# Performance work log

Hardware: AMD Instinct MI355X
Metric: run time of the kernel (lower is better)

## Reference

```python
import jax, jax.numpy as jnp
import numpy as np

SQRT_HALF = np.float32(np.sqrt(0.5))


def _weight_norm(v, g):
    # torch weight_norm dim=0: per-output-row normalization, w = g * v / ||v||_row
    return (g / jnp.linalg.norm(v, axis=1))[:, None] * v


def setup_inputs() -> dict:
    key = jax.random.key(0)
    ks = jax.random.split(key, 6)
    B, L, C, E, H, W = 32, 1024, 1024, 1024, 14, 14
    return {
        "x": jax.random.normal(ks[0], (B, L, C), dtype=jnp.float32),
        "word_embed": jax.random.normal(ks[1], (B, L, E), dtype=jnp.float32),
        "conv_feats": jax.random.normal(ks[2], (B, E, H, W), dtype=jnp.float32),
        "in_v": jax.random.normal(ks[3], (E, C), dtype=jnp.float32) * np.float32(1.0 / np.sqrt(C)),
        "in_g": jnp.ones((E,), dtype=jnp.float32),
        "in_b": jnp.zeros((E,), dtype=jnp.float32),
        "out_v": jax.random.normal(ks[4], (C, E), dtype=jnp.float32) * np.float32(1.0 / np.sqrt(E)),
        "out_g": jnp.ones((C,), dtype=jnp.float32),
        "out_b": jnp.zeros((C,), dtype=jnp.float32),
    }


def reference(x, word_embed, conv_feats, in_v, in_g, in_b, out_v, out_g, out_b):
    # in_projection (weight-normed linear) + word_embed, scaled
    Wi = _weight_norm(in_v, in_g)                      # [E, C]
    h = (jnp.einsum('blc,ec->ble', x, Wi) + in_b + word_embed) * SQRT_HALF  # [B, L, E]

    B, E, H, W = conv_feats.shape
    n = H * W
    y = conv_feats.reshape(B, E, n)                    # [B, E, n]
    scores = jnp.einsum('ble,bev->blv', h, y)          # [B, L, n]
    attn = jax.nn.softmax(scores, axis=-1)             # [B, L, n]
    ctx = jnp.einsum('blv,bev->ble', attn, y)          # [B, L, E]
    ctx = ctx * jnp.asarray(n * np.sqrt(1.0 / n), dtype=ctx.dtype)  # = sqrt(n)

    # out_projection + residual, scaled
    Wo = _weight_norm(out_v, out_g)                    # [C, E]
    out = (jnp.einsum('ble,ce->blc', ctx, Wo) + out_b + x) * SQRT_HALF  # [B, L, C]
    return out, attn
```

## Files before the change

### kernel.cpp

```cpp
#include <hip/hip_runtime.h>
#include <hip/hip_bf16.h>

typedef unsigned short u16;
typedef __bf16 bf16x8 __attribute__((ext_vector_type(8)));
typedef _Float16 f16x8 __attribute__((ext_vector_type(8)));
typedef unsigned short u16x8 __attribute__((ext_vector_type(8)));
typedef float f32x4 __attribute__((ext_vector_type(4)));

#define SQHF 0.70710678118654752440f

__device__ __forceinline__ u16 f2bf(float f) {
  __hip_bfloat16 h = __float2bfloat16(f);
  return __builtin_bit_cast(u16, h);
}
__device__ __forceinline__ float bf2f(u16 u) {
  unsigned x = ((unsigned)u) << 16;
  return __builtin_bit_cast(float, x);
}
__device__ __forceinline__ void split2(float v, u16& hi, u16& lo) {
  hi = f2bf(v);
  lo = f2bf(v - bf2f(hi));
}

template <int N>
__device__ __forceinline__ void vmwait() {
  asm volatile("s_waitcnt vmcnt(%0)" ::"i"(N) : "memory");
}

__device__ __forceinline__ void gload_lds16(const void* g, void* l) {
  __builtin_amdgcn_global_load_lds(
      (const __attribute__((address_space(1))) unsigned int*)g,
      (__attribute__((address_space(3))) unsigned int*)l, 16, 0, 0);
}

__device__ __forceinline__ float block_sum(float v) {
#pragma unroll
  for (int o = 32; o; o >>= 1) v += __shfl_xor(v, o);
  __shared__ float red[4];
  if ((threadIdx.x & 63) == 0) red[threadIdx.x >> 6] = v;
  __syncthreads();
  return red[0] + red[1] + red[2] + red[3];
}

__global__ void wnorm_t_kernel(const float* __restrict__ v, const float* __restrict__ g,
                               u16* __restrict__ wth, u16* __restrict__ wtl) {
  const int e = blockIdx.x;
  const float* vr = v + (long)e * 1024;
  float ss = 0.f;
  for (int c = threadIdx.x; c < 1024; c += 256) { float t = vr[c]; ss += t * t; }
  const float tot = block_sum(ss);
  const float scl = g[e] / sqrtf(tot);
  for (int c = threadIdx.x; c < 1024; c += 256) {
    u16 hi, lo;
    split2(vr[c] * scl, hi, lo);
    wth[(long)c * 1024 + e] = hi;
    wtl[(long)c * 1024 + e] = lo;
  }
}

__global__ void wnorm_kernel(const float* __restrict__ v, const float* __restrict__ g,
                             u16* __restrict__ w) {
  const int c = blockIdx.x;
  const float* vr = v + (long)c * 1024;
  float ss = 0.f;
  for (int e = threadIdx.x; e < 1024; e += 256) { float t = vr[e]; ss += t * t; }
  const float tot = block_sum(ss);
  const float scl = g[c] / sqrtf(tot);
  for (int e = threadIdx.x; e < 1024; e += 256) w[(long)c * 1024 + e] = f2bf(vr[e] * scl);
}

__global__ void prep_y_kernel(const float* __restrict__ conv, u16* __restrict__ bth,
                              u16* __restrict__ btl, u16* __restrict__ concat) {
  const int b = blockIdx.x >> 4;
  const int e0 = (blockIdx.x & 15) << 6;
  __shared__ float tile[64 * 224];
  const float* cb = conv + ((long)b * 1024 + e0) * 196;
  for (int idx = threadIdx.x; idx < 64 * 224; idx += 256) {
    const int rr = idx / 224, vv = idx - rr * 224;
    tile[idx] = (vv < 196) ? cb[(long)rr * 196 + vv] : 0.f;
  }
  __syncthreads();
  for (int idx = threadIdx.x; idx < 256 * 64; idx += 256) {
    const int vr = idx >> 6, c = idx & 63;
    const float val = (vr < 224) ? tile[c * 224 + vr] : 0.f;
    u16 hi, lo;
    split2(val, hi, lo);
    const long o = ((long)b * 256 + vr) * 1024 + e0 + c;
    bth[o] = hi;
    btl[o] = lo;
    const _Float16 hf = (_Float16)val;
    concat[((long)b * 256 + vr) * 2048 + 1024 + e0 + c] = __builtin_bit_cast(u16, hf);
  }
}

__global__ void rc_kernel(const float* __restrict__ in_b, const u16* __restrict__ bth,
                          const u16* __restrict__ btl, float* __restrict__ rc) {
  const int b = blockIdx.x / 49;
  const int v = (blockIdx.x % 49) * 4 + (threadIdx.x >> 6);
  const int lane = threadIdx.x & 63;
  const long base = ((long)b * 256 + v) * 1024;
  float acc = 0.f;
  for (int e = lane; e < 1024; e += 64)
    acc += in_b[e] * (bf2f(bth[base + e]) + bf2f(btl[base + e]));
#pragma unroll
  for (int o = 32; o; o >>= 1) acc += __shfl_xor(acc, o);
  if (lane == 0) rc[b * 256 + v] = acc;
}

__global__ void softmax_kernel(const float* __restrict__ s0b, const float* __restrict__ s1b,
                               const float* __restrict__ rc,
                               float* __restrict__ attn, u16* __restrict__ attn_bf) {
  const long row = (long)blockIdx.x * 4 + (threadIdx.x >> 6);
  const int lane = threadIdx.x & 63;
  const int b = (int)(row >> 10);
  const float* s0 = s0b + row * 256;
  const float* s1 = s1b + row * 256;
  const float* rcb = rc + b * 256;
  float v0 = (s0[lane] + s1[lane] + rcb[lane]) * SQHF;
  float v1 = (s0[64 + lane] + s1[64 + lane] + rcb[64 + lane]) * SQHF;
  float v2 = (s0[128 + lane] + s1[128 + lane] + rcb[128 + lane]) * SQHF;
  float v3 = (lane < 4) ? (s0[192 + lane] + s1[192 + lane] + rcb[192 + lane]) * SQHF : -1e30f;
  float mx = fmaxf(fmaxf(v0, v1), fmaxf(v2, v3));
#pragma unroll
  for (int o = 32; o; o >>= 1) mx = fmaxf(mx, __shfl_xor(mx, o));
  const float e0 = __expf(v0 - mx), e1 = __expf(v1 - mx), e2 = __expf(v2 - mx);
  const float e3 = (lane < 4) ? __expf(v3 - mx) : 0.f;
  float sm = e0 + e1 + e2 + e3;
#pragma unroll
  for (int o = 32; o; o >>= 1) sm += __shfl_xor(sm, o);
  const float inv = 1.f / sm;
  float* arow = attn + row * 196;
  arow[lane] = e0 * inv;
  arow[64 + lane] = e1 * inv;
  arow[128 + lane] = e2 * inv;
  if (lane < 4) arow[192 + lane] = e3 * inv;
  u16* brow = attn_bf + row * 256;
  brow[lane] = f2bf(e0 * inv);
  brow[64 + lane] = f2bf(e1 * inv);
  brow[128 + lane] = f2bf(e2 * inv);
  brow[192 + lane] = (lane < 4) ? f2bf(e3 * inv) : (u16)0;
}

template <int EPI, int MODE>
__global__ __launch_bounds__(256) void gemm128(
    const u16* __restrict__ Ah, const u16* __restrict__ Al,
    const float* __restrict__ Af0, const float* __restrict__ Af1, int kSw,
    const u16* __restrict__ Bh, const u16* __restrict__ Bl,
    int N, int K, int ldA, int ldB, int ldOut,
    int mTilesPerBatch, long bStride, int aTilesMod, int kSplit2,
    const float* __restrict__ bias, const float* __restrict__ extra,
    float scale, void* __restrict__ out1, void* __restrict__ out2) {
  constexpr int SPLIT = (MODE == 1);
  constexpr int AF16 = (MODE == 2);
  constexpr int DEPTH = AF16 ? 3 : 2;
  constexpr int LPS = (MODE == 0) ? 4 : (MODE == 1 ? 8 : 6);
  constexpr int TAL = 4096;
  constexpr int TBH = (MODE == 0) ? 4096 : 8192;
  constexpr int TBL = 12288;
  constexpr int HSM = (MODE == 0) ? 8192 : (MODE == 1 ? 16384 : 12288);
  __shared__ __align__(16) u16 smem[HSM * DEPTH];

  int bid = blockIdx.x, nwg = gridDim.x, half = 0;
  if (kSplit2) { half = bid & 1; bid >>= 1; nwg >>= 1; }
  const int kOff = half << 10;

  const int numN = N >> 7;
  const int q = nwg >> 3, r = nwg & 7, xcd = bid & 7, l8 = bid >> 3;
  const int wg = (xcd < r ? xcd * (q + 1) : r * (q + 1) + (xcd - r) * q) + l8;
  const int mTile = wg / numN, nTile = wg - mTile * numN;
  const long rowBase = (long)mTile << 7;
  const int colBase = nTile << 7;
  const int aTile = aTilesMod ? (mTile % aTilesMod) : mTile;
  const long aRowBase = (long)aTile << 7;
  const long bOff = mTilesPerBatch ? (long)(mTile / mTilesPerBatch) * bStride : 0;

  const u16* Agh = AF16 ? nullptr : (Ah + aRowBase * ldA);
  const u16* Agl = SPLIT ? (Al + aRowBase * ldA) : nullptr;
  const u16* Bgh = Bh + bOff + (long)colBase * ldB;
  const u16* Bgl = SPLIT ? (Bl + bOff + (long)colBase * ldB) : nullptr;

  const int tid = threadIdx.x;
  const int wave = tid >> 6, lane = tid & 63;
  const int wr = wave >> 1, wc = wave & 1;
  const int sr = wave * 16 + (lane >> 2);
  const int scS = (((lane & 3) ^ ((sr >> 1) & 3)) << 3);
  const int lr = lane & 15;
  const int lk = (lane >> 4) << 3;

  f32x4 acc[4][4];
#pragma unroll
  for (int m = 0; m < 4; ++m)
#pragma unroll
    for (int n = 0; n < 4; ++n) acc[m][n] = f32x4{0.f, 0.f, 0.f, 0.f};

  auto stage = [&](int buf, int k0) {
    u16* sb = smem + buf * HSM;
    if (AF16) {
      const int gk = k0 + kOff;
      const float* As = (gk < kSw) ? (Af0 + aRowBase * (long)ldA + gk)
                                   : (Af1 + aRowBase * (long)ldA + (gk - kSw));
      const int rr = tid >> 3;
#pragma unroll
      for (int i = 0; i < 4; ++i) {
        const int row = i * 32 + rr;
        const int csw = (((tid & 7) ^ (row & 7)) << 2);
        gload_lds16(As + (long)row * ldA + csw, &sb[i * 2048 + wave * 512]);
      }
#pragma unroll
      for (int i = 0; i < 2; ++i) {
        const long ro = (long)(i * 64 + sr) * ldB + k0 + kOff + scS;
        gload_lds16(Bgh + ro, &sb[TBH + i * 2048 + wave * 512]);
      }
    } else {
#pragma unroll
      for (int i = 0; i < 2; ++i) {
        const long roA = (long)(i * 64 + sr) * ldA + k0 + scS;
        const long roB = (long)(i * 64 + sr) * ldB + k0 + scS;
        const int lo_ = i * 2048 + wave * 512;
        gload_lds16(Agh + roA, &sb[lo_]);
        gload_lds16(Bgh + roB, &sb[TBH + lo_]);
        if (SPLIT) {
          gload_lds16(Agl + roA, &sb[TAL + lo_]);
          gload_lds16(Bgl + roB, &sb[TBL + lo_]);
        }
      }
    }
  };

  auto compute = [&](int buf) {
    const u16* sb = smem + buf * HSM;
    if (AF16) {
      f16x8 fa[4], fb[4];
      const char* smemb = (const char*)sb;
#pragma unroll
      for (int m = 0; m < 4; ++m) {
        const int row = wr * 64 + m * 16 + lr;
        const int xr = (row & 7) << 4;
        const char* rp = smemb + row * 128;
        const f32x4 p0 = *(const f32x4*)(rp + ((lk << 2) ^ xr));
        const f32x4 p1 = *(const f32x4*)(rp + (((lk << 2) + 16) ^ xr));
        f16x8 va;
        va[0] = (_Float16)p0.x; va[1] = (_Float16)p0.y;
        va[2] = (_Float16)p0.z; va[3] = (_Float16)p0.w;
        va[4] = (_Float16)p1.x; va[5] = (_Float16)p1.y;
        va[6] = (_Float16)p1.z; va[7] = (_Float16)p1.w;
        fa[m] = va;
      }
#pragma unroll
      for (int n = 0; n < 4; ++n) {
        const int row = wc * 64 + n * 16 + lr;
        const int off = row * 32 + (((lane >> 4) ^ ((row >> 1) & 3)) << 3);
        fb[n] = __builtin_bit_cast(f16x8, *(const u16x8*)&sb[TBH + off]);
      }
      __builtin_amdgcn_s_setprio(1);
#pragma unroll
      for (int m = 0; m < 4; ++m)
#pragma unroll
        for (int n = 0; n < 4; ++n)
          acc[m][n] = __builtin_amdgcn_mfma_f32_16x16x32_f16(fa[m], fb[n], acc[m][n], 0, 0, 0);
      __builtin_amdgcn_s_setprio(0);
    } else {
      bf16x8 fah[4], fbh[4], fal[4], fbl[4];
#pragma unroll
      for (int m = 0; m < 4; ++m) {
        const int row = wr * 64 + m * 16 + lr;
        const int off = row * 32 + (((lane >> 4) ^ ((row >> 1) & 3)) << 3);
        fah[m] = __builtin_bit_cast(bf16x8, *(const u16x8*)&sb[off]);
        if (SPLIT) fal[m] = __builtin_bit_cast(bf16x8, *(const u16x8*)&sb[TAL + off]);
      }
#pragma unroll
      for (int n = 0; n < 4; ++n) {
        const int row = wc * 64 + n * 16 + lr;
        const int off = row * 32 + (((lane >> 4) ^ ((row >> 1) & 3)) << 3);
        fbh[n] = __builtin_bit_cast(bf16x8, *(const u16x8*)&sb[TBH + off]);
        if (SPLIT) fbl[n] = __builtin_bit_cast(bf16x8, *(const u16x8*)&sb[TBL + off]);
      }
#pragma unroll
      for (int m = 0; m < 4; ++m)
#pragma unroll
        for (int n = 0; n < 4; ++n) {
          acc[m][n] = __builtin_amdgcn_mfma_f32_16x16x32_bf16(fah[m], fbh[n], acc[m][n], 0, 0, 0);
          if (SPLIT) {
            acc[m][n] = __builtin_amdgcn_mfma_f32_16x16x32_bf16(fah[m], fbl[n], acc[m][n], 0, 0, 0);
            acc[m][n] = __builtin_amdgcn_mfma_f32_16x16x32_bf16(fal[m], fbh[n], acc[m][n], 0, 0, 0);
          }
        }
    }
  };

  const int nSteps = K >> 5;
  stage(0, 0);
  if (DEPTH == 3 && nSteps > 1) stage(1, 32);
  for (int t = 0; t < nSteps; ++t) {
    const int cur = t % DEPTH;
    if (t + DEPTH - 1 < nSteps) {
      stage((t + DEPTH - 1) % DEPTH, (t + DEPTH - 1) << 5);
      vmwait<LPS * (DEPTH - 1)>();
    } else if (DEPTH == 3 && t + 1 < nSteps) {
      vmwait<LPS>();
    } else {
      vmwait<0>();
    }
    __builtin_amdgcn_s_barrier();
    __builtin_amdgcn_sched_barrier(0);
    compute(cur);
    __builtin_amdgcn_sched_barrier(0);
    __builtin_amdgcn_s_barrier();
  }

  const int rloc = (lane >> 4) << 2;
  float* o3 = (float*)(half ? out2 : out1);
#pragma unroll
  for (int m = 0; m < 4; ++m) {
#pragma unroll
    for (int n = 0; n < 4; ++n) {
      const int col = colBase + wc * 64 + n * 16 + lr;
#pragma unroll
      for (int j = 0; j < 4; ++j) {
        const long row = rowBase + wr * 64 + m * 16 + rloc + j;
        const float v = acc[m][n][j];
        if (EPI == 1) {
          ((float*)out1)[row * (long)ldOut + col] =
              (v + bias[col] + extra[row * 1024 + col]) * scale;
        } else if (EPI == 2) {
          ((u16*)out1)[row * (long)ldOut + col] = f2bf(v * scale);
        } else if (EPI == 3) {
          o3[row * (long)ldOut + col] = v;
        } else if (EPI == 6) {
          const _Float16 hv = (_Float16)v;
          ((u16*)out1)[row * (long)ldOut + col] = __builtin_bit_cast(u16, hv);
        }
      }
    }
  }
}

extern "C" void kernel_launch(void* const* d_in, const int* in_sizes, int n_in,
                              void* d_out, int out_size, void* d_ws, size_t ws_size,
                              hipStream_t stream) {
  (void)in_sizes; (void)n_in; (void)out_size; (void)ws_size;
  const float* x     = (const float*)d_in[0];
  const float* we    = (const float*)d_in[1];
  const float* conv  = (const float*)d_in[2];
  const float* in_v  = (const float*)d_in[3];
  const float* in_g  = (const float*)d_in[4];
  const float* in_b  = (const float*)d_in[5];
  const float* out_v = (const float*)d_in[6];
  const float* out_g = (const float*)d_in[7];
  const float* out_b = (const float*)d_in[8];
  float* out  = (float*)d_out;
  float* attn = out + 33554432l;

  char* ws = (char*)d_ws;
  u16* bth    = (u16*)(ws);
  u16* btl    = (u16*)(ws + 16777216l);
  u16* concat = (u16*)(ws + 33554432l);
  u16* wth    = (u16*)(ws + 67108864l);
  u16* wtl    = (u16*)(ws + 69206016l);
  u16* wo     = (u16*)(ws + 71303168l);
  u16* zo     = (u16*)(ws + 73400320l);
  u16* attbf  = (u16*)(ws + 90177536l);
  float* rc   = (float*)(ws + 106954752l);
  float* s1   = (float*)(ws + 109051904l);
  float* s0   = out;

  wnorm_t_kernel<<<1024, 256, 0, stream>>>(in_v, in_g, wth, wtl);
  wnorm_kernel<<<1024, 256, 0, stream>>>(out_v, out_g, wo);
  prep_y_kernel<<<512, 256, 0, stream>>>(conv, bth, btl, concat);
  rc_kernel<<<1568, 256, 0, stream>>>(in_b, bth, btl, rc);
  gemm128<6, 1><<<512, 256, 0, stream>>>(
      bth, btl, nullptr, nullptr, 0, wth, wtl,
      1024, 1024, 1024, 1024, 2048, 0, 0, 0, 0, nullptr, nullptr, 1.f, concat, nullptr);
  gemm128<3, 2><<<1024, 256, 0, stream>>>(
      nullptr, nullptr, x, we, 1024, concat, nullptr,
      256, 1024, 1024, 2048, 256, 8, 524288l, 0, 1, nullptr, nullptr, 1.f, s0, s1);
  softmax_kernel<<<8192, 256, 0, stream>>>(s0, s1, rc, attn, attbf);
  gemm128<2, 0><<<512, 256, 0, stream>>>(
      wo, nullptr, nullptr, nullptr, 0, bth, nullptr,
      256, 1024, 1024, 1024, 256, 8, 262144l, 8, 0, nullptr, nullptr, 14.f, zo, nullptr);
  gemm128<1, 0><<<2048, 256, 0, stream>>>(
      attbf, nullptr, nullptr, nullptr, 0, zo, nullptr,
      1024, 256, 256, 256, 1024, 8, 262144l, 0, 0, out_b, x, SQHF, out, nullptr);
}
```

Baseline: 355.6 us.

## Switch all GEMMs to single-pass fp16 and fuse rc into prep kernel

Replaces the three-pass split-bf16 (hi/lo) emulation of fp32 in the y·Wi GEMM with a single fp16 MFMA pass. It also moves the remaining bf16 GEMMs to fp16 operands and reads the fp16 copy of conv features from the concat buffer, which drops the separate bth/btl buffers. The rc bias-dot kernel is folded into prep_y, accumulating with atomics into a zero-initialised buffer. This cuts MFMA work, memory traffic and one launch, at the cost of lower precision in the h-projection path and fp16 range risk.

Measured after the change: 302.1 us. 15.1% less time.

```diff
diff --git a/kernel.cpp b/kernel.cpp
--- a/kernel.cpp
+++ b/kernel.cpp
@@ -2,24 +2,15 @@
 #include <hip/hip_bf16.h>
 
 typedef unsigned short u16;
-typedef __bf16 bf16x8 __attribute__((ext_vector_type(8)));
 typedef _Float16 f16x8 __attribute__((ext_vector_type(8)));
 typedef unsigned short u16x8 __attribute__((ext_vector_type(8)));
 typedef float f32x4 __attribute__((ext_vector_type(4)));
 
 #define SQHF 0.70710678118654752440f
 
-__device__ __forceinline__ u16 f2bf(float f) {
-  __hip_bfloat16 h = __float2bfloat16(f);
+__device__ __forceinline__ u16 f2h(float f) {
+  const _Float16 h = (_Float16)f;
   return __builtin_bit_cast(u16, h);
-}
-__device__ __forceinline__ float bf2f(u16 u) {
-  unsigned x = ((unsigned)u) << 16;
-  return __builtin_bit_cast(float, x);
-}
-__device__ __forceinline__ void split2(float v, u16& hi, u16& lo) {
-  hi = f2bf(v);
-  lo = f2bf(v - bf2f(hi));
 }
 
 template <int N>
@@ -43,19 +34,14 @@
 }
 
 __global__ void wnorm_t_kernel(const float* __restrict__ v, const float* __restrict__ g,
-                               u16* __restrict__ wth, u16* __restrict__ wtl) {
+                               u16* __restrict__ wtf) {
   const int e = blockIdx.x;
   const float* vr = v + (long)e * 1024;
   float ss = 0.f;
   for (int c = threadIdx.x; c < 1024; c += 256) { float t = vr[c]; ss += t * t; }
   const float tot = block_sum(ss);
   const float scl = g[e] / sqrtf(tot);
-  for (int c = threadIdx.x; c < 1024; c += 256) {
-    u16 hi, lo;
-    split2(vr[c] * scl, hi, lo);
-    wth[(long)c * 1024 + e] = hi;
-    wtl[(long)c * 1024 + e] = lo;
-  }
+  for (int c = threadIdx.x; c < 1024; c += 256) wtf[(long)c * 1024 + e] = f2h(vr[c] * scl);
 }
 
 __global__ void wnorm_kernel(const float* __restrict__ v, const float* __restrict__ g,
@@ -66,11 +52,11 @@
   for (int e = threadIdx.x; e < 1024; e += 256) { float t = vr[e]; ss += t * t; }
   const float tot = block_sum(ss);
   const float scl = g[c] / sqrtf(tot);
-  for (int e = threadIdx.x; e < 1024; e += 256) w[(long)c * 1024 + e] = f2bf(vr[e] * scl);
-}
-
-__global__ void prep_y_kernel(const float* __restrict__ conv, u16* __restrict__ bth,
-                              u16* __restrict__ btl, u16* __restrict__ concat) {
+  for (int e = threadIdx.x; e < 1024; e += 256) w[(long)c * 1024 + e] = f2h(vr[e] * scl);
+}
+
+__global__ void prep_y_kernel(const float* __restrict__ conv, const float* __restrict__ in_b,
+                              u16* __restrict__ concat, float* __restrict__ rc) {
   const int b = blockIdx.x >> 4;
   const int e0 = (blockIdx.x & 15) << 6;
   __shared__ float tile[64 * 224];
@@ -83,33 +69,20 @@
   for (int idx = threadIdx.x; idx < 256 * 64; idx += 256) {
     const int vr = idx >> 6, c = idx & 63;
     const float val = (vr < 224) ? tile[c * 224 + vr] : 0.f;
-    u16 hi, lo;
-    split2(val, hi, lo);
-    const long o = ((long)b * 256 + vr) * 1024 + e0 + c;
-    bth[o] = hi;
-    btl[o] = lo;
-    const _Float16 hf = (_Float16)val;
-    concat[((long)b * 256 + vr) * 2048 + 1024 + e0 + c] = __builtin_bit_cast(u16, hf);
-  }
-}
-
-__global__ void rc_kernel(const float* __restrict__ in_b, const u16* __restrict__ bth,
-                          const u16* __restrict__ btl, float* __restrict__ rc) {
-  const int b = blockIdx.x / 49;
-  const int v = (blockIdx.x % 49) * 4 + (threadIdx.x >> 6);
-  const int lane = threadIdx.x & 63;
-  const long base = ((long)b * 256 + v) * 1024;
-  float acc = 0.f;
-  for (int e = lane; e < 1024; e += 64)
-    acc += in_b[e] * (bf2f(bth[base + e]) + bf2f(btl[base + e]));
-#pragma unroll
-  for (int o = 32; o; o >>= 1) acc += __shfl_xor(acc, o);
-  if (lane == 0) rc[b * 256 + v] = acc;
+    concat[((long)b * 256 + vr) * 2048 + 1024 + e0 + c] = f2h(val);
+  }
+  const int v = threadIdx.x;
+  if (v < 196) {
+    float s = 0.f;
+#pragma unroll 8
+    for (int rr = 0; rr < 64; ++rr) s += in_b[e0 + rr] * tile[rr * 224 + v];
+    atomicAdd(&rc[b * 256 + v], s);
+  }
 }
 
 __global__ void softmax_kernel(const float* __restrict__ s0b, const float* __restrict__ s1b,
                                const float* __restrict__ rc,
-                               float* __restrict__ attn, u16* __restrict__ attn_bf) {
+                               float* __restrict__ attn, u16* __restrict__ attn_f) {
   const long row = (long)blockIdx.x * 4 + (threadIdx.x >> 6);
   const int lane = threadIdx.x & 63;
   const int b = (int)(row >> 10);
@@ -134,31 +107,27 @@
   arow[64 + lane] = e1 * inv;
   arow[128 + lane] = e2 * inv;
   if (lane < 4) arow[192 + lane] = e3 * inv;
-  u16* brow = attn_bf + row * 256;
-  brow[lane] = f2bf(e0 * inv);
-  brow[64 + lane] = f2bf(e1 * inv);
-  brow[128 + lane] = f2bf(e2 * inv);
-  brow[192 + lane] = (lane < 4) ? f2bf(e3 * inv) : (u16)0;
+  u16* brow = attn_f + row * 256;
+  brow[lane] = f2h(e0 * inv);
+  brow[64 + lane] = f2h(e1 * inv);
+  brow[128 + lane] = f2h(e2 * inv);
+  brow[192 + lane] = (lane < 4) ? f2h(e3 * inv) : (u16)0;
 }
 
 template <int EPI, int MODE>
 __global__ __launch_bounds__(256) void gemm128(
-    const u16* __restrict__ Ah, const u16* __restrict__ Al,
+    const u16* __restrict__ Ah,
     const float* __restrict__ Af0, const float* __restrict__ Af1, int kSw,
-    const u16* __restrict__ Bh, const u16* __restrict__ Bl,
+    const u16* __restrict__ Bh,
     int N, int K, int ldA, int ldB, int ldOut,
     int mTilesPerBatch, long bStride, int aTilesMod, int kSplit2,
     const float* __restrict__ bias, const float* __restrict__ extra,
     float scale, void* __restrict__ out1, void* __restrict__ out2) {
-  constexpr int SPLIT = (MODE == 1);
-  constexpr int AF16 = (MODE == 2);
-  constexpr int DEPTH = AF16 ? 3 : 2;
-  constexpr int LPS = (MODE == 0) ? 4 : (MODE == 1 ? 8 : 6);
-  constexpr int TAL = 4096;
-  constexpr int TBH = (MODE == 0) ? 4096 : 8192;
-  constexpr int TBL = 12288;
-  constexpr int HSM = (MODE == 0) ? 8192 : (MODE == 1 ? 16384 : 12288);
-  __shared__ __align__(16) u16 smem[HSM * DEPTH];
+  constexpr int AF32 = (MODE == 2);
+  constexpr int LPS = AF32 ? 6 : 4;
+  constexpr int TBH = AF32 ? 8192 : 4096;
+  constexpr int HSM = AF32 ? 12288 : 8192;
+  __shared__ __align__(16) u16 smem[HSM * 2];
 
   int bid = blockIdx.x, nwg = gridDim.x, half = 0;
   if (kSplit2) { half = bid & 1; bid >>= 1; nwg >>= 1; }
@@ -174,10 +143,8 @@
   const long aRowBase = (long)aTile << 7;
   const long bOff = mTilesPerBatch ? (long)(mTile / mTilesPerBatch) * bStride : 0;
 
-  const u16* Agh = AF16 ? nullptr : (Ah + aRowBase * ldA);
-  const u16* Agl = SPLIT ? (Al + aRowBase * ldA) : nullptr;
+  const u16* Agh = AF32 ? nullptr : (Ah + aRowBase * ldA);
   const u16* Bgh = Bh + bOff + (long)colBase * ldB;
-  const u16* Bgl = SPLIT ? (Bl + bOff + (long)colBase * ldB) : nullptr;
 
   const int tid = threadIdx.x;
   const int wave = tid >> 6, lane = tid & 63;
@@ -195,7 +162,7 @@
 
   auto stage = [&](int buf, int k0) {
     u16* sb = smem + buf * HSM;
-    if (AF16) {
+    if (AF32) {
       const int gk = k0 + kOff;
       const float* As = (gk < kSw) ? (Af0 + aRowBase * (long)ldA + gk)
                                    : (Af1 + aRowBase * (long)ldA + (gk - kSw));
@@ -214,23 +181,19 @@
     } else {
 #pragma unroll
       for (int i = 0; i < 2; ++i) {
-        const long roA = (long)(i * 64 + sr) * ldA + k0 + scS;
-        const long roB = (long)(i * 64 + sr) * ldB + k0 + scS;
+        const long roA = (long)(i * 64 + sr) * ldA + k0 + kOff + scS;
+        const long roB = (long)(i * 64 + sr) * ldB + k0 + kOff + scS;
         const int lo_ = i * 2048 + wave * 512;
         gload_lds16(Agh + roA, &sb[lo_]);
         gload_lds16(Bgh + roB, &sb[TBH + lo_]);
-        if (SPLIT) {
-          gload_lds16(Agl + roA, &sb[TAL + lo_]);
-          gload_lds16(Bgl + roB, &sb[TBL + lo_]);
-        }
       }
     }
   };
 
   auto compute = [&](int buf) {
     const u16* sb = smem + buf * HSM;
-    if (AF16) {
-      f16x8 fa[4], fb[4];
+    f16x8 fa[4], fb[4];
+    if (AF32) {
       const char* smemb = (const char*)sb;
 #pragma unroll
       for (int m = 0; m < 4; ++m) {
@@ -246,57 +209,35 @@
         va[6] = (_Float16)p1.z; va[7] = (_Float16)p1.w;
         fa[m] = va;
       }
-#pragma unroll
-      for (int n = 0; n < 4; ++n) {
-        const int row = wc * 64 + n * 16 + lr;
-        const int off = row * 32 + (((lane >> 4) ^ ((row >> 1) & 3)) << 3);
-        fb[n] = __builtin_bit_cast(f16x8, *(const u16x8*)&sb[TBH + off]);
-      }
-      __builtin_amdgcn_s_setprio(1);
-#pragma unroll
-      for (int m = 0; m < 4; ++m)
-#pragma unroll
-        for (int n = 0; n < 4; ++n)
-          acc[m][n] = __builtin_amdgcn_mfma_f32_16x16x32_f16(fa[m], fb[n], acc[m][n], 0, 0, 0);
-      __builtin_amdgcn_s_setprio(0);
     } else {
-      bf16x8 fah[4], fbh[4], fal[4], fbl[4];
 #pragma unroll
       for (int m = 0; m < 4; ++m) {
         const int row = wr * 64 + m * 16 + lr;
         const int off = row * 32 + (((lane >> 4) ^ ((row >> 1) & 3)) << 3);
-        fah[m] = __builtin_bit_cast(bf16x8, *(const u16x8*)&sb[off]);
-        if (SPLIT) fal[m] = __builtin_bit_cast(bf16x8, *(const u16x8*)&sb[TAL + off]);
-      }
-#pragma unroll
-      for (int n = 0; n < 4; ++n) {
-        const int row = wc * 64 + n * 16 + lr;
-        const int off = row * 32 + (((lane >> 4) ^ ((row >> 1) & 3)) << 3);
-        fbh[n] = __builtin_bit_cast(bf16x8, *(const u16x8*)&sb[TBH + off]);
-        if (SPLIT) fbl[n] = __builtin_bit_cast(bf16x8, *(const u16x8*)&sb[TBL + off]);
-      }
-#pragma unroll
-      for (int m = 0; m < 4; ++m)
-#pragma unroll
-        for (int n = 0; n < 4; ++n) {
-          acc[m][n] = __builtin_amdgcn_mfma_f32_16x16x32_bf16(fah[m], fbh[n], acc[m][n], 0, 0, 0);
-          if (SPLIT) {
-            acc[m][n] = __builtin_amdgcn_mfma_f32_16x16x32_bf16(fah[m], fbl[n], acc[m][n], 0, 0, 0);
-            acc[m][n] = __builtin_amdgcn_mfma_f32_16x16x32_bf16(fal[m], fbh[n], acc[m][n], 0, 0, 0);
-          }
-        }
-    }
+        fa[m] = __builtin_bit_cast(f16x8, *(const u16x8*)&sb[off]);
+      }
+    }
+#pragma unroll
+    for (int n = 0; n < 4; ++n) {
+      const int row = wc * 64 + n * 16 + lr;
+      const int off = row * 32 + (((lane >> 4) ^ ((row >> 1) & 3)) << 3);
+      fb[n] = __builtin_bit_cast(f16x8, *(const u16x8*)&sb[TBH + off]);
+    }
+    __builtin_amdgcn_s_setprio(1);
+#pragma unroll
+    for (int m = 0; m < 4; ++m)
+#pragma unroll
+      for (int n = 0; n < 4; ++n)
+        acc[m][n] = __builtin_amdgcn_mfma_f32_16x16x32_f16(fa[m], fb[n], acc[m][n], 0, 0, 0);
+    __builtin_amdgcn_s_setprio(0);
   };
 
   const int nSteps = K >> 5;
   stage(0, 0);
-  if (DEPTH == 3 && nSteps > 1) stage(1, 32);
   for (int t = 0; t < nSteps; ++t) {
-    const int cur = t % DEPTH;
-    if (t + DEPTH - 1 < nSteps) {
-      stage((t + DEPTH - 1) % DEPTH, (t + DEPTH - 1) << 5);
-      vmwait<LPS * (DEPTH - 1)>();
-    } else if (DEPTH == 3 && t + 1 < nSteps) {
+    const int cur = t & 1;
+    if (t + 1 < nSteps) {
+      stage(cur ^ 1, (t + 1) << 5);
       vmwait<LPS>();
     } else {
       vmwait<0>();
@@ -321,14 +262,11 @@
         const float v = acc[m][n][j];
         if (EPI == 1) {
           ((float*)out1)[row * (long)ldOut + col] =
-              (v + bias[col] + extra[row * 1024 + col]) * scale;
-        } else if (EPI == 2) {
-          ((u16*)out1)[row * (long)ldOut + col] = f2bf(v * scale);
+              (v + bias[col] + extra[row * (long)ldOut + col]) * scale;
         } else if (EPI == 3) {
           o3[row * (long)ldOut + col] = v;
         } else if (EPI == 6) {
-          const _Float16 hv = (_Float16)v;
-          ((u16*)out1)[row * (long)ldOut + col] = __builtin_bit_cast(u16, hv);
+          ((u16*)out1)[row * (long)ldOut + col] = f2h(v * scale);
         }
       }
     }
@@ -352,33 +290,30 @@
   float* attn = out + 33554432l;
 
   char* ws = (char*)d_ws;
-  u16* bth    = (u16*)(ws);
-  u16* btl    = (u16*)(ws + 16777216l);
-  u16* concat = (u16*)(ws + 33554432l);
-  u16* wth    = (u16*)(ws + 67108864l);
-  u16* wtl    = (u16*)(ws + 69206016l);
-  u16* wo     = (u16*)(ws + 71303168l);
-  u16* zo     = (u16*)(ws + 73400320l);
-  u16* attbf  = (u16*)(ws + 90177536l);
-  float* rc   = (float*)(ws + 106954752l);
-  float* s1   = (float*)(ws + 109051904l);
+  u16* concat = (u16*)(ws);
+  u16* wtf    = (u16*)(ws + 33554432l);
+  u16* wo     = (u16*)(ws + 35651584l);
+  u16* zo     = (u16*)(ws + 37748736l);
+  u16* attf   = (u16*)(ws + 54525952l);
+  float* rc   = (float*)(ws + 71303168l);
+  float* s1   = (float*)(ws + 71368704l);
   float* s0   = out;
 
-  wnorm_t_kernel<<<1024, 256, 0, stream>>>(in_v, in_g, wth, wtl);
+  hipMemsetAsync(rc, 0, 32 * 256 * sizeof(float), stream);
+  wnorm_t_kernel<<<1024, 256, 0, stream>>>(in_v, in_g, wtf);
   wnorm_kernel<<<1024, 256, 0, stream>>>(out_v, out_g, wo);
-  prep_y_kernel<<<512, 256, 0, stream>>>(conv, bth, btl, concat);
-  rc_kernel<<<1568, 256, 0, stream>>>(in_b, bth, btl, rc);
-  gemm128<6, 1><<<512, 256, 0, stream>>>(
-      bth, btl, nullptr, nullptr, 0, wth, wtl,
-      1024, 1024, 1024, 1024, 2048, 0, 0, 0, 0, nullptr, nullptr, 1.f, concat, nullptr);
+  prep_y_kernel<<<512, 256, 0, stream>>>(conv, in_b, concat, rc);
+  gemm128<6, 3><<<512, 256, 0, stream>>>(
+      concat + 1024, nullptr, nullptr, 0, wtf,
+      1024, 1024, 2048, 1024, 2048, 0, 0, 0, 0, nullptr, nullptr, 1.f, concat, nullptr);
   gemm128<3, 2><<<1024, 256, 0, stream>>>(
-      nullptr, nullptr, x, we, 1024, concat, nullptr,
+      nullptr, x, we, 1024, concat,
       256, 1024, 1024, 2048, 256, 8, 524288l, 0, 1, nullptr, nullptr, 1.f, s0, s1);
-  softmax_kernel<<<8192, 256, 0, stream>>>(s0, s1, rc, attn, attbf);
-  gemm128<2, 0><<<512, 256, 0, stream>>>(
-      wo, nullptr, nullptr, nullptr, 0, bth, nullptr,
-      256, 1024, 1024, 1024, 256, 8, 262144l, 8, 0, nullptr, nullptr, 14.f, zo, nullptr);
-  gemm128<1, 0><<<2048, 256, 0, stream>>>(
-      attbf, nullptr, nullptr, nullptr, 0, zo, nullptr,
+  softmax_kernel<<<8192, 256, 0, stream>>>(s0, s1, rc, attn, attf);
+  gemm128<6, 3><<<512, 256, 0, stream>>>(
+      wo, nullptr, nullptr, 0, concat + 1024,
+      256, 1024, 1024, 2048, 256, 8, 524288l, 8, 0, nullptr, nullptr, 14.f, zo, nullptr);
+  gemm128<1, 3><<<2048, 256, 0, stream>>>(
+      attf, nullptr, nullptr, 0, zo,
       1024, 256, 256, 256, 1024, 8, 262144l, 0, 0, out_b, x, SQHF, out, nullptr);
 }
```
